# Optimization experiments

Hardware: AMD Instinct MI355X
Metric: run time of the kernel (lower is better)

Reference implementation:

```python
import jax, jax.numpy as jnp
import numpy as np

N, C, O, R, T, V = 128, 64, 64, 8, 128, 25  # batch, in_ch, out_ch, rel_ch, frames, joints
EPS = 1e-5


def _c1(x, w, b):
    # 1x1 conv2d over channel dim: x [n,i,t,v], w [o,i], b [o]
    return jnp.einsum('oi,nitv->notv', w, x) + b[None, :, None, None]


def _tconv(x, w):
    # temporal conv, kernel [3,1], pad [1,0]: x [n,c,t,1], w [o,i,3,1]
    return jax.lax.conv_general_dilated(
        x, w, window_strides=(1, 1), padding=((1, 1), (0, 0)),
        dimension_numbers=('NCHW', 'OIHW', 'NCHW'))


def setup_inputs() -> dict:
    key = jax.random.key(0)
    ks = jax.random.split(key, 16)
    d = {}
    d['x'] = jax.random.normal(ks[0], (N, C, T, V), jnp.float32)
    d['A'] = jax.random.normal(ks[1], (V, V), jnp.float32) * 0.1
    d['alpha'] = jnp.ones((1,), jnp.float32)
    s_c = 1.0 / np.sqrt(C)
    s_r = 1.0 / np.sqrt(R)
    d['w1'] = jax.random.normal(ks[2], (R, C), jnp.float32) * s_c
    d['b1'] = jnp.zeros((R,), jnp.float32)
    d['w2'] = jax.random.normal(ks[3], (R, C), jnp.float32) * s_c
    d['b2'] = jnp.zeros((R,), jnp.float32)
    d['w5'] = jax.random.normal(ks[4], (R, C), jnp.float32) * s_c
    d['b5'] = jnp.zeros((R,), jnp.float32)
    d['w3'] = jax.random.normal(ks[5], (O, R), jnp.float32) * s_r
    d['b3'] = jnp.zeros((O,), jnp.float32)
    d['w4'] = jax.random.normal(ks[6], (O, R), jnp.float32) * s_r
    d['b4'] = jnp.zeros((O,), jnp.float32)
    # RouteFuncMLP params (ratio=1, kernels=[3,3])
    d['g_w'] = jax.random.normal(ks[7], (R, R), jnp.float32) * s_r
    d['g_b'] = jnp.zeros((R,), jnp.float32)
    d['a_w'] = jax.random.normal(ks[8], (R, R, 3, 1), jnp.float32) * s_r
    d['a_b'] = jnp.zeros((R,), jnp.float32)
    d['bn_g'] = jnp.ones((R,), jnp.float32)
    d['bn_b'] = jnp.zeros((R,), jnp.float32)
    d['bn_rm'] = jnp.zeros((R,), jnp.float32)
    d['bn_rv'] = jnp.ones((R,), jnp.float32)
    # conv_rf.b is zero-init in torch (trivial gate); randomize small for a meaningful test
    d['rf_bw'] = jax.random.normal(ks[9], (R, R, 3, 1), jnp.float32) * 0.05
    return d


def reference(x, A, alpha, w1, b1, w2, b2, w5, b5, w3, b3, w4, b4,
              g_w, g_b, a_w, a_b, bn_g, bn_b, bn_rm, bn_rv, rf_bw):
    # x1, x2: 1x1 conv then mean over T  -> [N,R,V]
    x1 = _c1(x, w1, b1).mean(axis=2)
    x2 = _c1(x, w2, b2).mean(axis=2)
    x3 = _c1(x, w5, b5)  # [N,R,T,V]

    # RouteFuncMLP gating on x3
    g = x3.mean(axis=(2, 3), keepdims=True)          # global pool [N,R,1,1]
    p = x3.mean(axis=3, keepdims=True)               # pool over V [N,R,T,1]
    gg = _c1(g, g_w, g_b)                            # 1x1 conv on global pool
    h = _tconv(p + gg, a_w) + a_b[None, :, None, None]
    h = (h - bn_rm[None, :, None, None]) * (bn_g / jnp.sqrt(bn_rv + EPS))[None, :, None, None] + bn_b[None, :, None, None]
    h = jax.nn.relu(h)
    rf = _tconv(h, rf_bw) + 1.0                      # [N,R,T,1]

    x3 = _c1(x3 * rf, w3, b3)                        # [N,O,T,V]

    # relation tensor: broadcast diff + tanh -> [N,R,V,V]
    rel = jnp.tanh(x1[:, :, :, None] - x2[:, :, None, :])
    rel = _c1(rel, w4, b4) * alpha[0] + A[None, None]  # [N,O,V,V]

    # aggregation: out[n,c,t,u] = sum_v rel[n,c,u,v] * x3[n,c,t,v]
    out = jnp.einsum('ncuv,nctv->nctu', rel, x3)
    return out
```

## Files before the change

kernel.cpp:

```cpp
#include <hip/hip_runtime.h>

#define N_ 128
#define C_ 64
#define O_ 64
#define R_ 8
#define T_ 128
#define V_ 25
#define TV_ 3200
#define EPS_ 1e-5f
#define G_ 4

__global__ __launch_bounds__(256) void k1_colsum(const float* __restrict__ x,
                                                 float* __restrict__ S) {
    int ni = blockIdx.x;
    const float* xp = x + (size_t)ni * TV_;
    int tid = threadIdx.x;
    __shared__ float part[200];
    if (tid < 200) {
        float s = 0.f;
        #pragma unroll
        for (int k = 0; k < 16; ++k) s += xp[tid + 200 * k];
        part[tid] = s;
    }
    __syncthreads();
    if (tid < V_) {
        float t = 0.f;
        #pragma unroll
        for (int g = 0; g < 8; ++g) t += part[g * 25 + tid];
        S[ni * V_ + tid] = t;
    }
}

__global__ __launch_bounds__(256) void k3_x3(const float* __restrict__ x,
        const float* __restrict__ w5, const float* __restrict__ b5,
        float* __restrict__ x3) {
    __shared__ float w5s[R_ * C_];
    int tid = threadIdx.x;
    w5s[tid] = w5[tid];
    w5s[tid + 256] = w5[tid + 256];
    __syncthreads();
    int gid = blockIdx.x * 256 + tid;
    int n = gid / TV_, p = gid % TV_;
    float acc[R_];
    #pragma unroll
    for (int r = 0; r < R_; ++r) acc[r] = b5[r];
    const float* xp = x + (size_t)n * C_ * TV_ + p;
    for (int i = 0; i < C_; ++i) {
        float xv = xp[(size_t)i * TV_];
        #pragma unroll
        for (int r = 0; r < R_; ++r) acc[r] += w5s[r * C_ + i] * xv;
    }
    float* x3p = x3 + (size_t)n * R_ * TV_ + p;
    #pragma unroll
    for (int r = 0; r < R_; ++r) x3p[(size_t)r * TV_] = acc[r];
}

__global__ __launch_bounds__(256) void kP_pool(const float* __restrict__ x3,
                                               float* __restrict__ ppool) {
    int nr = blockIdx.x;
    int tid = threadIdx.x;
    __shared__ float buf[TV_];
    const float* xp = x3 + (size_t)nr * TV_;
    for (int idx = tid; idx < TV_; idx += 256) buf[idx] = xp[idx];
    __syncthreads();
    if (tid < T_) {
        float s = 0.f;
        #pragma unroll
        for (int v = 0; v < V_; ++v) s += buf[tid * V_ + v];
        ppool[(size_t)nr * T_ + tid] = s;
    }
}

__global__ __launch_bounds__(256) void k2_rel(const float* __restrict__ S,
        const float* __restrict__ w1, const float* __restrict__ b1,
        const float* __restrict__ w2, const float* __restrict__ b2,
        const float* __restrict__ w4, const float* __restrict__ b4,
        const float* __restrict__ A, const float* __restrict__ alpha,
        float* __restrict__ rel2) {
    int n = blockIdx.x, og = blockIdx.y;
    int c0 = og * 16;
    int tid = threadIdx.x;
    __shared__ float x1s[R_ * V_];
    __shared__ float x2s[R_ * V_];
    __shared__ float rels[R_ * 625];
    const float invT = 1.0f / (float)T_;
    for (int idx = tid; idx < 2 * R_ * V_; idx += 256) {
        int s = idx / (R_ * V_), rv = idx % (R_ * V_);
        int r = rv / V_, v = rv % V_;
        const float* w = s ? w2 : w1;
        float a = 0.f;
        for (int i = 0; i < C_; ++i) a += w[r * C_ + i] * S[(n * C_ + i) * V_ + v];
        a = a * invT + (s ? b2[r] : b1[r]);
        (s ? x2s : x1s)[rv] = a;
    }
    __syncthreads();
    for (int idx = tid; idx < R_ * 625; idx += 256) {
        int r = idx / 625, uv = idx % 625;
        rels[idx] = tanhf(x1s[r * V_ + uv / V_] - x2s[r * V_ + uv % V_]);
    }
    __syncthreads();
    float al = alpha[0];
    for (int idx = tid; idx < 16 * 625; idx += 256) {
        int o = c0 + idx / 625, uv = idx % 625;
        float acc = b4[o];
        #pragma unroll
        for (int r = 0; r < R_; ++r) acc += w4[o * R_ + r] * rels[r * 625 + uv];
        rel2[((size_t)n * O_ + o) * 625 + uv] = acc * al + A[uv];
    }
}

__global__ __launch_bounds__(256) void k4_route(const float* __restrict__ ppool,
        const float* __restrict__ g_w, const float* __restrict__ g_b,
        const float* __restrict__ a_w, const float* __restrict__ a_b,
        const float* __restrict__ bn_g, const float* __restrict__ bn_b,
        const float* __restrict__ bn_rm, const float* __restrict__ bn_rv,
        const float* __restrict__ rf_bw, float* __restrict__ rf) {
    int n = blockIdx.x, tid = threadIdx.x;
    __shared__ float ps[R_][T_];
    __shared__ float hs[R_][T_];
    __shared__ float gs[R_];
    __shared__ float ggs[R_];
    for (int idx = tid; idx < R_ * T_; idx += 256)
        ps[idx / T_][idx % T_] = ppool[(size_t)n * R_ * T_ + idx] * (1.0f / V_);
    __syncthreads();
    if (tid < R_) {
        float s = 0.f;
        for (int t = 0; t < T_; ++t) s += ps[tid][t];
        gs[tid] = s * (1.0f / T_);
    }
    __syncthreads();
    if (tid < R_) {
        float a = g_b[tid];
        #pragma unroll
        for (int i = 0; i < R_; ++i) a += g_w[tid * R_ + i] * gs[i];
        ggs[tid] = a;
    }
    __syncthreads();
    for (int idx = tid; idx < R_ * T_; idx += 256) {
        int r = idx / T_, t = idx % T_;
        float acc = a_b[r];
        #pragma unroll
        for (int i = 0; i < R_; ++i) {
            #pragma unroll
            for (int k = 0; k < 3; ++k) {
                int tt = t + k - 1;
                if (tt >= 0 && tt < T_)
                    acc += a_w[(r * R_ + i) * 3 + k] * (ps[i][tt] + ggs[i]);
            }
        }
        float sc = bn_g[r] * rsqrtf(bn_rv[r] + EPS_);
        float h = (acc - bn_rm[r]) * sc + bn_b[r];
        hs[r][t] = fmaxf(h, 0.f);
    }
    __syncthreads();
    for (int idx = tid; idx < R_ * T_; idx += 256) {
        int r = idx / T_, t = idx % T_;
        float acc = 1.0f;
        #pragma unroll
        for (int i = 0; i < R_; ++i) {
            #pragma unroll
            for (int k = 0; k < 3; ++k) {
                int tt = t + k - 1;
                if (tt >= 0 && tt < T_)
                    acc += rf_bw[(r * R_ + i) * 3 + k] * hs[i][tt];
            }
        }
        rf[((size_t)n * R_ + r) * T_ + t] = acc;
    }
}

__global__ __launch_bounds__(256) void k5_out(const float* __restrict__ x3,
        const float* __restrict__ rf, const float* __restrict__ rel2,
        const float* __restrict__ w3, const float* __restrict__ b3,
        float* __restrict__ out) {
    int b = blockIdx.x;
    int n = b / 32;
    int rem = b % 32;
    int cg = rem / 2, th = rem % 2;
    int c0 = cg * G_;
    int tid = threadIdx.x;
    __shared__ float rfs[R_][T_ / 2];
    __shared__ float zs[G_][1600];
    __shared__ float rels[G_][625];
    for (int idx = tid; idx < R_ * (T_ / 2); idx += 256) {
        int r = idx / (T_ / 2), tt = idx % (T_ / 2);
        rfs[r][tt] = rf[((size_t)n * R_ + r) * T_ + th * (T_ / 2) + tt];
    }
    for (int idx = tid; idx < G_ * 625; idx += 256)
        rels[idx / 625][idx % 625] = rel2[((size_t)n * O_ + c0 + idx / 625) * 625 + idx % 625];
    float w3s[G_][R_], b3s[G_];
    #pragma unroll
    for (int cl = 0; cl < G_; ++cl) {
        b3s[cl] = b3[c0 + cl];
        #pragma unroll
        for (int r = 0; r < R_; ++r) w3s[cl][r] = w3[(c0 + cl) * R_ + r];
    }
    __syncthreads();
    const float* x3p = x3 + (size_t)n * R_ * TV_ + th * 1600;
    for (int p = tid; p < 1600; p += 256) {
        int t = p / V_;
        float xv[R_];
        #pragma unroll
        for (int r = 0; r < R_; ++r) xv[r] = x3p[(size_t)r * TV_ + p] * rfs[r][t];
        #pragma unroll
        for (int cl = 0; cl < G_; ++cl) {
            float acc = b3s[cl];
            #pragma unroll
            for (int r = 0; r < R_; ++r) acc += w3s[cl][r] * xv[r];
            zs[cl][p] = acc;
        }
    }
    __syncthreads();
    float* op = out + (((size_t)n * O_ + c0) * T_ + th * (T_ / 2)) * V_;
    for (int cl = 0; cl < G_; ++cl) {
        const float* zrow = zs[cl];
        const float* rrow = rels[cl];
        for (int idx = tid; idx < 1600; idx += 256) {
            int t = idx / V_, u = idx % V_;
            float acc = 0.f;
            #pragma unroll
            for (int v = 0; v < V_; ++v) acc += zrow[t * V_ + v] * rrow[u * V_ + v];
            op[(size_t)cl * T_ * V_ + idx] = acc;
        }
    }
}

extern "C" void kernel_launch(void* const* d_in, const int* in_sizes, int n_in,
                              void* d_out, int out_size, void* d_ws, size_t ws_size,
                              hipStream_t stream) {
    const float* x     = (const float*)d_in[0];
    const float* A     = (const float*)d_in[1];
    const float* alpha = (const float*)d_in[2];
    const float* w1    = (const float*)d_in[3];
    const float* b1    = (const float*)d_in[4];
    const float* w2    = (const float*)d_in[5];
    const float* b2    = (const float*)d_in[6];
    const float* w5    = (const float*)d_in[7];
    const float* b5    = (const float*)d_in[8];
    const float* w3    = (const float*)d_in[9];
    const float* b3    = (const float*)d_in[10];
    const float* w4    = (const float*)d_in[11];
    const float* b4    = (const float*)d_in[12];
    const float* g_w   = (const float*)d_in[13];
    const float* g_b   = (const float*)d_in[14];
    const float* a_w   = (const float*)d_in[15];
    const float* a_b   = (const float*)d_in[16];
    const float* bn_g  = (const float*)d_in[17];
    const float* bn_b  = (const float*)d_in[18];
    const float* bn_rm = (const float*)d_in[19];
    const float* bn_rv = (const float*)d_in[20];
    const float* rf_bw = (const float*)d_in[21];
    float* out = (float*)d_out;
    float* ws  = (float*)d_ws;

    float* S     = ws;
    float* x3    = S + 204800;
    float* ppool = x3 + 3276800;
    float* rf    = ppool + 131072;
    float* rel2  = rf + 131072;

    hipLaunchKernelGGL(k1_colsum, dim3(N_ * C_), dim3(256), 0, stream, x, S);
    hipLaunchKernelGGL(k3_x3, dim3(1600), dim3(256), 0, stream, x, w5, b5, x3);
    hipLaunchKernelGGL(kP_pool, dim3(N_ * R_), dim3(256), 0, stream, x3, ppool);
    hipLaunchKernelGGL(k2_rel, dim3(N_, 4), dim3(256), 0, stream,
                       S, w1, b1, w2, b2, w4, b4, A, alpha, rel2);
    hipLaunchKernelGGL(k4_route, dim3(N_), dim3(256), 0, stream,
                       ppool, g_w, g_b, a_w, a_b, bn_g, bn_b, bn_rm, bn_rv, rf_bw, rf);
    hipLaunchKernelGGL(k5_out, dim3(N_ * 32), dim3(256), 0, stream,
                       x3, rf, rel2, w3, b3, out);
}
```

Baseline: 359.3 us.

## Register-block aggregation in output kernel and fuse V-pooling into route kernel

The output kernel now processes 8 channels per 512-thread block. Each thread keeps a row of 25 z values in registers and reads the padded relation matrix as float4, which cuts repeated shared-memory reads in the V×V aggregation. Results are staged back through LDS so the global stores stay coalesced. The separate pooling kernel is removed and the route kernel sums x3 over joints directly, saving a launch and an intermediate buffer. k3 reads w5 from global memory with a fully unrolled loop instead of staging it in LDS. The trade-off is higher register and LDS use per block, which lowers occupancy.

```diff
diff --git a/kernel.cpp b/kernel.cpp
--- a/kernel.cpp
+++ b/kernel.cpp
@@ -8,7 +8,7 @@
 #define V_ 25
 #define TV_ 3200
 #define EPS_ 1e-5f
-#define G_ 4
+#define G_ 8
 
 __global__ __launch_bounds__(256) void k1_colsum(const float* __restrict__ x,
                                                  float* __restrict__ S) {
@@ -34,41 +34,21 @@
 __global__ __launch_bounds__(256) void k3_x3(const float* __restrict__ x,
         const float* __restrict__ w5, const float* __restrict__ b5,
         float* __restrict__ x3) {
-    __shared__ float w5s[R_ * C_];
-    int tid = threadIdx.x;
-    w5s[tid] = w5[tid];
-    w5s[tid + 256] = w5[tid + 256];
-    __syncthreads();
-    int gid = blockIdx.x * 256 + tid;
+    int gid = blockIdx.x * 256 + threadIdx.x;
     int n = gid / TV_, p = gid % TV_;
     float acc[R_];
     #pragma unroll
     for (int r = 0; r < R_; ++r) acc[r] = b5[r];
     const float* xp = x + (size_t)n * C_ * TV_ + p;
+    #pragma unroll
     for (int i = 0; i < C_; ++i) {
         float xv = xp[(size_t)i * TV_];
         #pragma unroll
-        for (int r = 0; r < R_; ++r) acc[r] += w5s[r * C_ + i] * xv;
+        for (int r = 0; r < R_; ++r) acc[r] += w5[r * C_ + i] * xv;
     }
     float* x3p = x3 + (size_t)n * R_ * TV_ + p;
     #pragma unroll
     for (int r = 0; r < R_; ++r) x3p[(size_t)r * TV_] = acc[r];
-}
-
-__global__ __launch_bounds__(256) void kP_pool(const float* __restrict__ x3,
-                                               float* __restrict__ ppool) {
-    int nr = blockIdx.x;
-    int tid = threadIdx.x;
-    __shared__ float buf[TV_];
-    const float* xp = x3 + (size_t)nr * TV_;
-    for (int idx = tid; idx < TV_; idx += 256) buf[idx] = xp[idx];
-    __syncthreads();
-    if (tid < T_) {
-        float s = 0.f;
-        #pragma unroll
-        for (int v = 0; v < V_; ++v) s += buf[tid * V_ + v];
-        ppool[(size_t)nr * T_ + tid] = s;
-    }
 }
 
 __global__ __launch_bounds__(256) void k2_rel(const float* __restrict__ S,
@@ -109,7 +89,7 @@
     }
 }
 
-__global__ __launch_bounds__(256) void k4_route(const float* __restrict__ ppool,
+__global__ __launch_bounds__(256) void k4_route(const float* __restrict__ x3,
         const float* __restrict__ g_w, const float* __restrict__ g_b,
         const float* __restrict__ a_w, const float* __restrict__ a_b,
         const float* __restrict__ bn_g, const float* __restrict__ bn_b,
@@ -120,8 +100,14 @@
     __shared__ float hs[R_][T_];
     __shared__ float gs[R_];
     __shared__ float ggs[R_];
-    for (int idx = tid; idx < R_ * T_; idx += 256)
-        ps[idx / T_][idx % T_] = ppool[(size_t)n * R_ * T_ + idx] * (1.0f / V_);
+    for (int idx = tid; idx < R_ * T_; idx += 256) {
+        int r = idx / T_, t = idx % T_;
+        const float* xp = x3 + ((size_t)n * R_ + r) * TV_ + t * V_;
+        float s = 0.f;
+        #pragma unroll
+        for (int v = 0; v < V_; ++v) s += xp[v];
+        ps[r][t] = s * (1.0f / V_);
+    }
     __syncthreads();
     if (tid < R_) {
         float s = 0.f;
@@ -169,59 +155,72 @@
     }
 }
 
-__global__ __launch_bounds__(256) void k5_out(const float* __restrict__ x3,
+__global__ __launch_bounds__(512) void k5_out(const float* __restrict__ x3,
         const float* __restrict__ rf, const float* __restrict__ rel2,
         const float* __restrict__ w3, const float* __restrict__ b3,
         float* __restrict__ out) {
     int b = blockIdx.x;
-    int n = b / 32;
-    int rem = b % 32;
+    int n = b / 16;
+    int rem = b % 16;
     int cg = rem / 2, th = rem % 2;
     int c0 = cg * G_;
     int tid = threadIdx.x;
-    __shared__ float rfs[R_][T_ / 2];
+    __shared__ float rfs[R_][64];
     __shared__ float zs[G_][1600];
-    __shared__ float rels[G_][625];
-    for (int idx = tid; idx < R_ * (T_ / 2); idx += 256) {
-        int r = idx / (T_ / 2), tt = idx % (T_ / 2);
-        rfs[r][tt] = rf[((size_t)n * R_ + r) * T_ + th * (T_ / 2) + tt];
-    }
-    for (int idx = tid; idx < G_ * 625; idx += 256)
-        rels[idx / 625][idx % 625] = rel2[((size_t)n * O_ + c0 + idx / 625) * 625 + idx % 625];
-    float w3s[G_][R_], b3s[G_];
-    #pragma unroll
-    for (int cl = 0; cl < G_; ++cl) {
-        b3s[cl] = b3[c0 + cl];
-        #pragma unroll
-        for (int r = 0; r < R_; ++r) w3s[cl][r] = w3[(c0 + cl) * R_ + r];
+    __shared__ float rels[G_][V_][28];
+    if (tid < R_ * 64) {
+        int r = tid / 64, tl = tid % 64;
+        rfs[r][tl] = rf[((size_t)n * R_ + r) * T_ + th * 64 + tl];
+    }
+    for (int idx = tid; idx < G_ * 625; idx += 512) {
+        int cl = idx / 625, uv = idx % 625;
+        rels[cl][uv / 25][uv % 25] = rel2[((size_t)n * O_ + c0 + cl) * 625 + uv];
     }
     __syncthreads();
     const float* x3p = x3 + (size_t)n * R_ * TV_ + th * 1600;
-    for (int p = tid; p < 1600; p += 256) {
+    for (int p = tid; p < 1600; p += 512) {
         int t = p / V_;
-        float xv[R_];
-        #pragma unroll
-        for (int r = 0; r < R_; ++r) xv[r] = x3p[(size_t)r * TV_ + p] * rfs[r][t];
+        float y[R_];
+        #pragma unroll
+        for (int r = 0; r < R_; ++r) y[r] = x3p[(size_t)r * TV_ + p] * rfs[r][t];
         #pragma unroll
         for (int cl = 0; cl < G_; ++cl) {
-            float acc = b3s[cl];
+            float a = b3[c0 + cl];
             #pragma unroll
-            for (int r = 0; r < R_; ++r) acc += w3s[cl][r] * xv[r];
-            zs[cl][p] = acc;
-        }
-    }
-    __syncthreads();
-    float* op = out + (((size_t)n * O_ + c0) * T_ + th * (T_ / 2)) * V_;
-    for (int cl = 0; cl < G_; ++cl) {
-        const float* zrow = zs[cl];
-        const float* rrow = rels[cl];
-        for (int idx = tid; idx < 1600; idx += 256) {
-            int t = idx / V_, u = idx % V_;
-            float acc = 0.f;
-            #pragma unroll
-            for (int v = 0; v < V_; ++v) acc += zrow[t * V_ + v] * rrow[u * V_ + v];
-            op[(size_t)cl * T_ * V_ + idx] = acc;
-        }
+            for (int r = 0; r < R_; ++r) a += w3[(c0 + cl) * R_ + r] * y[r];
+            zs[cl][p] = a;
+        }
+    }
+    __syncthreads();
+    {
+        int cl = tid >> 6, tl = tid & 63;
+        float zreg[V_];
+        #pragma unroll
+        for (int v = 0; v < V_; ++v) zreg[v] = zs[cl][tl * V_ + v];
+        float accu[V_];
+        #pragma unroll
+        for (int u = 0; u < V_; ++u) {
+            const float4* rp4 = (const float4*)&rels[cl][u][0];
+            float4 a0 = rp4[0], a1 = rp4[1], a2 = rp4[2];
+            float4 a3 = rp4[3], a4 = rp4[4], a5 = rp4[5];
+            float acc = zreg[24] * rels[cl][u][24];
+            acc += zreg[0] * a0.x + zreg[1] * a0.y + zreg[2] * a0.z + zreg[3] * a0.w;
+            acc += zreg[4] * a1.x + zreg[5] * a1.y + zreg[6] * a1.z + zreg[7] * a1.w;
+            acc += zreg[8] * a2.x + zreg[9] * a2.y + zreg[10] * a2.z + zreg[11] * a2.w;
+            acc += zreg[12] * a3.x + zreg[13] * a3.y + zreg[14] * a3.z + zreg[15] * a3.w;
+            acc += zreg[16] * a4.x + zreg[17] * a4.y + zreg[18] * a4.z + zreg[19] * a4.w;
+            acc += zreg[20] * a5.x + zreg[21] * a5.y + zreg[22] * a5.z + zreg[23] * a5.w;
+            accu[u] = acc;
+        }
+        #pragma unroll
+        for (int u = 0; u < V_; ++u) zs[cl][tl * V_ + u] = accu[u];
+    }
+    __syncthreads();
+    size_t ob = (((size_t)n * O_ + c0) * T_ + th * 64) * V_;
+    const float* zf = &zs[0][0];
+    for (int j = tid; j < G_ * 1600; j += 512) {
+        int cl = j / 1600, rest = j % 1600;
+        out[ob + (size_t)cl * (T_ * V_) + rest] = zf[j];
     }
 }
 
@@ -255,17 +254,15 @@
 
     float* S     = ws;
     float* x3    = S + 204800;
-    float* ppool = x3 + 3276800;
-    float* rf    = ppool + 131072;
+    float* rf    = x3 + 3276800;
     float* rel2  = rf + 131072;
 
     hipLaunchKernelGGL(k1_colsum, dim3(N_ * C_), dim3(256), 0, stream, x, S);
     hipLaunchKernelGGL(k3_x3, dim3(1600), dim3(256), 0, stream, x, w5, b5, x3);
-    hipLaunchKernelGGL(kP_pool, dim3(N_ * R_), dim3(256), 0, stream, x3, ppool);
     hipLaunchKernelGGL(k2_rel, dim3(N_, 4), dim3(256), 0, stream,
                        S, w1, b1, w2, b2, w4, b4, A, alpha, rel2);
     hipLaunchKernelGGL(k4_route, dim3(N_), dim3(256), 0, stream,
-                       ppool, g_w, g_b, a_w, a_b, bn_g, bn_b, bn_rm, bn_rv, rf_bw, rf);
-    hipLaunchKernelGGL(k5_out, dim3(N_ * 32), dim3(256), 0, stream,
+                       x3, g_w, g_b, a_w, a_b, bn_g, bn_b, bn_rm, bn_rv, rf_bw, rf);
+    hipLaunchKernelGGL(k5_out, dim3(N_ * 16), dim3(512), 0, stream,
                        x3, rf, rel2, w3, b3, out);
 }
```

Result: faster. 322.7 us (-10.2%).
